# Kernel optimization log

Hardware: AMD Instinct MI355X
Metric: run time of the kernel (lower is better)

The kernel has to match this reference:

```python
import jax, jax.numpy as jnp
import numpy as np

N, L, DS, DP, H, A, Q, V = 1, 512, 384, 256, 12, 16, 4, 8
SHID = H * (DP + A + 3 * V + V)  # 3648
WC = float(np.sqrt(2.0 / (9.0 * Q)))
WL = float(np.sqrt(1.0 / 3.0))
EPS = 1e-5


def quat2rot(q):
    # q: (..., 3) partial quaternion (w fixed to 1, then normalized) -> (..., 3, 3)
    ones = jnp.ones(q.shape[:-1] + (1,), q.dtype)
    qf = jnp.concatenate([ones, q], axis=-1)
    qf = qf / jnp.linalg.norm(qf, axis=-1, keepdims=True)
    w, x, y, z = qf[..., 0], qf[..., 1], qf[..., 2], qf[..., 3]
    r0 = jnp.stack([1 - 2 * (y * y + z * z), 2 * (x * y - w * z), 2 * (x * z + w * y)], -1)
    r1 = jnp.stack([2 * (x * y + w * z), 1 - 2 * (x * x + z * z), 2 * (y * z - w * x)], -1)
    r2 = jnp.stack([2 * (x * z - w * y), 2 * (y * z + w * x), 1 - 2 * (x * x + y * y)], -1)
    return jnp.stack([r0, r1, r2], axis=-2)


def layer_norm(x, g, b):
    m = x.mean(-1, keepdims=True)
    v = ((x - m) ** 2).mean(-1, keepdims=True)
    return (x - m) / jnp.sqrt(v + EPS) * g + b


def setup_inputs() -> dict:
    key = jax.random.key(0)
    ks = jax.random.split(key, 24)
    w = lambda k, shape, s=0.02: (jax.random.normal(k, shape, jnp.float32) * s)
    return {
        'sfea': jax.random.normal(ks[0], (N, L, DS), jnp.float32),
        'pfea': jax.random.normal(ks[1], (N, L, L, DP), jnp.float32),
        'quat': jax.random.normal(ks[2], (N, L, 3), jnp.float32) * 0.1,
        'trsl': jax.random.normal(ks[3], (N, L, 3), jnp.float32),
        'Wq': w(ks[4], (DS, H * A)), 'Wk': w(ks[5], (DS, H * A)), 'Wv': w(ks[6], (DS, H * A)),
        'Wqp': w(ks[7], (DS, H * Q * 3)), 'Wkp': w(ks[8], (DS, H * Q * 3)), 'Wvp': w(ks[9], (DS, H * V * 3)),
        'Wb': w(ks[10], (DP, H)),
        'scale': jnp.ones((H,), jnp.float32),
        'Ws': w(ks[11], (SHID, DS)), 'bs': jnp.zeros((DS,), jnp.float32),
        'W1': w(ks[12], (DS, DS)), 'b1': jnp.zeros((DS,), jnp.float32),
        'W2': w(ks[13], (DS, DS)), 'b2': jnp.zeros((DS,), jnp.float32),
        'W3': w(ks[14], (DS, DS)), 'b3': jnp.zeros((DS,), jnp.float32),
        'g1': jnp.ones((DS,), jnp.float32), 'be1': jnp.zeros((DS,), jnp.float32),
        'g2': jnp.ones((DS,), jnp.float32), 'be2': jnp.zeros((DS,), jnp.float32),
    }


def reference(sfea, pfea, quat, trsl, Wq, Wk, Wv, Wqp, Wkp, Wvp, Wb, scale, Ws, bs,
              W1, b1, W2, b2, W3, b3, g1, be1, g2, be2):
    n, l = sfea.shape[0], sfea.shape[1]
    # projections
    q = (sfea @ Wq).reshape(n, l, H, A)
    k = (sfea @ Wk).reshape(n, l, H, A)
    v = (sfea @ Wv).reshape(n, l, H, A)
    qp = (sfea @ Wqp).reshape(n, l, H, Q, 3)
    kp = (sfea @ Wkp).reshape(n, l, H, Q, 3)
    vp = (sfea @ Wvp).reshape(n, l, H, V, 3)
    b = jnp.einsum('nijp,ph->nijh', pfea, Wb)
    # local frames
    rot = quat2rot(quat)  # (n, l, 3, 3)
    t = trsl[:, :, None, None, :]
    qp_g = jnp.einsum('nlij,nlhqj->nlhqi', rot, qp) + t
    kp_g = jnp.einsum('nlij,nlhqj->nlhqi', rot, kp) + t
    vp_g = jnp.einsum('nlij,nlhvj->nlhvi', rot, vp) + t
    # attention logits
    qk = jnp.einsum('nihd,njhd->nijh', q, k) / np.sqrt(A)
    diff = qp_g[:, :, None] - kp_g[:, None]  # (n, i, j, h, q, 3)
    d2 = jnp.sum(diff * diff, axis=(-1, -2))  # (n, i, j, h)
    qkp = (WC * jax.nn.softplus(scale) / 2.0) * d2
    a = jax.nn.softmax(WL * (qk + b - qkp), axis=2)  # (n, i, j, h)
    # weighted sums (einsum avoids huge broadcast intermediates)
    op = jnp.einsum('nijh,nijp->nihp', a, pfea)
    ov = jnp.einsum('nijh,njhd->nihd', a, v)
    ovp_g = jnp.einsum('nijh,njhvc->nihvc', a, vp_g)
    # map back into local frame: R^T (x - t)
    ovp = jnp.einsum('nlji,nlhvj->nlhvi', rot, ovp_g - t)
    ovp_norm = jnp.sqrt(jnp.sum(ovp * ovp, axis=-1))  # (n, l, h, v)
    shid = jnp.concatenate([op, ov, ovp.reshape(n, l, H, V * 3), ovp_norm], axis=-1)
    shid = shid.reshape(n, l, SHID)
    # output projection + residual, post-LN, MLP, post-LN (v1 path, p_drop=0)
    s = sfea + shid @ Ws + bs
    s = layer_norm(s, g1, be1)
    h = jax.nn.relu(s @ W1 + b1)
    h = jax.nn.relu(h @ W2 + b2)
    s = s + (h @ W3 + b3)
    s = layer_norm(s, g2, be2)
    return s
```

## Files before the change

### kernel.cpp

```cpp
#include <hip/hip_runtime.h>
#include <cstddef>

typedef __attribute__((ext_vector_type(8))) short short8;
typedef __attribute__((ext_vector_type(4))) float f32x4;

#define WC_CONST 0.2357022603955158f
#define WL_CONST 0.5773502691896258f

__device__ __forceinline__ unsigned short rne_bf16(float f) {
  unsigned int u = __float_as_uint(f);
  u += 0x7fffu + ((u >> 16) & 1u);
  return (unsigned short)(u >> 16);
}

__global__ __launch_bounds__(256) void concat_w_kernel(
    const float* __restrict__ Wq, const float* __restrict__ Wk, const float* __restrict__ Wv,
    const float* __restrict__ Wqp, const float* __restrict__ Wkp, const float* __restrict__ Wvp,
    float* __restrict__ Wcat) {
  int idx = blockIdx.x * 256 + threadIdx.x;
  if (idx >= 384 * 1152) return;
  int k = idx / 1152, c = idx % 1152;
  float v;
  if (c < 192)       v = Wq [k*192 + c];
  else if (c < 384)  v = Wk [k*192 + (c-192)];
  else if (c < 576)  v = Wv [k*192 + (c-384)];
  else if (c < 720)  v = Wqp[k*144 + (c-576)];
  else if (c < 864)  v = Wkp[k*144 + (c-720)];
  else               v = Wvp[k*288 + (c-864)];
  Wcat[idx] = v;
}

__global__ __launch_bounds__(256) void gemm64_kernel(
    const float* __restrict__ Amat, const float* __restrict__ Bmat, float* __restrict__ Cp,
    int M, int N, int K, int ksl) {
  __shared__ float As[16][68];
  __shared__ float Bs[16][68];
  int t = threadIdx.x;
  int bn = blockIdx.x, bm = blockIdx.y, bz = blockIdx.z;
  int k0 = bz * ksl;
  int tr = t >> 4, tc = t & 15;
  int lm = t >> 2, lk4 = (t & 3) << 2;
  int lkb = t >> 4, lnq = (t & 15) << 2;
  const float* Ab = Amat + (size_t)(bm*64 + lm) * K;
  const float* Bb = Bmat + bn*64 + lnq;
  float acc[4][4];
  #pragma unroll
  for (int a2 = 0; a2 < 4; a2++)
    #pragma unroll
    for (int b2 = 0; b2 < 4; b2++) acc[a2][b2] = 0.f;

  for (int k = k0; k < k0 + ksl; k += 16) {
    float4 av = *(const float4*)(Ab + k + lk4);
    float4 bv = *(const float4*)(Bb + (size_t)(k + lkb) * N);
    As[lk4+0][lm] = av.x; As[lk4+1][lm] = av.y; As[lk4+2][lm] = av.z; As[lk4+3][lm] = av.w;
    *(float4*)&Bs[lkb][lnq] = bv;
    __syncthreads();
    #pragma unroll
    for (int kk = 0; kk < 16; kk++) {
      float4 a4 = *(const float4*)&As[kk][tr << 2];
      float4 b4 = *(const float4*)&Bs[kk][tc << 2];
      float ar[4] = {a4.x, a4.y, a4.z, a4.w};
      float br[4] = {b4.x, b4.y, b4.z, b4.w};
      #pragma unroll
      for (int a2 = 0; a2 < 4; a2++)
        #pragma unroll
        for (int b2 = 0; b2 < 4; b2++) acc[a2][b2] += ar[a2] * br[b2];
    }
    __syncthreads();
  }
  float* Cb = Cp + (size_t)bz * M * N + (size_t)(bm*64 + (tr << 2)) * N + bn*64 + (tc << 2);
  #pragma unroll
  for (int r = 0; r < 4; r++) {
    float4 o = {acc[r][0], acc[r][1], acc[r][2], acc[r][3]};
    *(float4*)(Cb + (size_t)r * N) = o;
  }
}

__global__ __launch_bounds__(256) void reduce_kernel(
    const float* __restrict__ Cp, float* __restrict__ out, const float* __restrict__ bias,
    int relu, int MN, int N, int sk) {
  int idx = blockIdx.x * 256 + threadIdx.x;
  if (idx >= MN) return;
  float s = 0.f;
  for (int z = 0; z < sk; z++) s += Cp[(size_t)z * MN + idx];
  if (bias) s += bias[idx % N];
  if (relu) s = fmaxf(s, 0.f);
  out[idx] = s;
}

__global__ __launch_bounds__(64) void frames_kernel(
    const float* __restrict__ proj, const float* __restrict__ quat, const float* __restrict__ trsl,
    float* __restrict__ rotb, float* __restrict__ qpg, float* __restrict__ kpg,
    float* __restrict__ vpg) {
  int i = blockIdx.x, t = threadIdx.x;
  float q0 = quat[i*3+0], q1 = quat[i*3+1], q2 = quat[i*3+2];
  float inv = rsqrtf(1.f + q0*q0 + q1*q1 + q2*q2);
  float w = inv, x = q0*inv, y = q1*inv, z = q2*inv;
  float R00 = 1.f - 2.f*(y*y + z*z), R01 = 2.f*(x*y - w*z), R02 = 2.f*(x*z + w*y);
  float R10 = 2.f*(x*y + w*z), R11 = 1.f - 2.f*(x*x + z*z), R12 = 2.f*(y*z - w*x);
  float R20 = 2.f*(x*z - w*y), R21 = 2.f*(y*z + w*x), R22 = 1.f - 2.f*(x*x + y*y);
  float t0 = trsl[i*3+0], t1 = trsl[i*3+1], t2 = trsl[i*3+2];
  if (t == 0) {
    float* rb = rotb + i*9;
    rb[0]=R00; rb[1]=R01; rb[2]=R02; rb[3]=R10; rb[4]=R11; rb[5]=R12; rb[6]=R20; rb[7]=R21; rb[8]=R22;
  }
  for (int pt = t; pt < 192; pt += 64) {
    const float* src; float* dst;
    if (pt < 48)      { src = proj + i*1152 + 576 + pt*3;        dst = qpg + i*144 + pt*3; }
    else if (pt < 96) { src = proj + i*1152 + 720 + (pt-48)*3;   dst = kpg + i*144 + (pt-48)*3; }
    else              { src = proj + i*1152 + 864 + (pt-96)*3;   dst = vpg + i*288 + (pt-96)*3; }
    float p0 = src[0], p1 = src[1], p2 = src[2];
    dst[0] = R00*p0 + R01*p1 + R02*p2 + t0;
    dst[1] = R10*p0 + R11*p1 + R12*p2 + t1;
    dst[2] = R20*p0 + R21*p1 + R22*p2 + t2;
  }
}

__global__ __launch_bounds__(256) void b_mfma_kernel(
    const float* __restrict__ pfea, const float* __restrict__ Wb, float* __restrict__ bmat) {
  __shared__ short wbf[8][64][8];
  int t = threadIdx.x;
  for (int s = t; s < 512; s += 256) {
    int ks = s >> 6, l = s & 63;
    int col = l & 15, kb = ks * 32 + ((l >> 4) << 3);
    #pragma unroll
    for (int j = 0; j < 8; j++)
      wbf[ks][l][j] = (col < 12) ? (short)rne_bf16(Wb[(kb + j) * 12 + col]) : (short)0;
  }
  __syncthreads();
  int wv = t >> 6, lane = t & 63;
  int wglob = blockIdx.x * 4 + wv;
  int row = lane & 15, kq = lane >> 4;
  for (int it = 0; it < 4; it++) {
    int tile = wglob * 4 + it;
    size_t p0 = (size_t)tile * 16;
    const float* Ab = pfea + (p0 + row) * 256 + kq * 8;
    f32x4 acc = {0.f, 0.f, 0.f, 0.f};
    #pragma unroll
    for (int ks = 0; ks < 8; ks++) {
      float4 f0 = *(const float4*)(Ab + ks * 32);
      float4 f1 = *(const float4*)(Ab + ks * 32 + 4);
      short8 af;
      af[0] = (short)rne_bf16(f0.x); af[1] = (short)rne_bf16(f0.y);
      af[2] = (short)rne_bf16(f0.z); af[3] = (short)rne_bf16(f0.w);
      af[4] = (short)rne_bf16(f1.x); af[5] = (short)rne_bf16(f1.y);
      af[6] = (short)rne_bf16(f1.z); af[7] = (short)rne_bf16(f1.w);
      short8 bfv = *(const short8*)(&wbf[ks][lane][0]);
      acc = __builtin_amdgcn_mfma_f32_16x16x32_bf16(af, bfv, acc, 0, 0, 0);
    }
    int col = lane & 15;
    if (col < 12) {
      #pragma unroll
      for (int r = 0; r < 4; r++) {
        size_t pr = p0 + kq * 4 + r;
        bmat[pr * 12 + col] = acc[r];
      }
    }
  }
}

__global__ __launch_bounds__(768) void attn_kernel(
    const float* __restrict__ proj, const float* __restrict__ qpg,
    const float* __restrict__ kpg, const float* __restrict__ vpg,
    const float* __restrict__ bmat, const float* __restrict__ pfea,
    const float* __restrict__ rotb, const float* __restrict__ trsl,
    const float* __restrict__ scale, float* __restrict__ shid) {
  int i = blockIdx.x;
  int t = threadIdx.x;
  __shared__ float Ll[12][512];
  __shared__ float qs[12][16];
  __shared__ float qps[12][12];
  __shared__ float coefs[12];
  __shared__ float ovpg_l[12][24];
  __shared__ float rot_s[9];

  for (int idx = t; idx < 192; idx += 768) qs[idx >> 4][idx & 15] = proj[i*1152 + idx];
  for (int idx = t; idx < 144; idx += 768) qps[idx / 12][idx % 12] = qpg[i*144 + idx];
  if (t < 12) coefs[t] = WC_CONST * 0.5f * log1pf(__expf(scale[t]));
  if (t < 9)  rot_s[t] = rotb[i*9 + t];
  __syncthreads();

  for (int idx = t; idx < 6144; idx += 768) {
    int h = idx % 12, j = idx / 12;
    const float4* kr = (const float4*)(proj + j*1152 + 192 + h*16);
    const float4* qr = (const float4*)(&qs[h][0]);
    float qk = 0.f;
    #pragma unroll
    for (int m = 0; m < 4; m++) {
      float4 kv = kr[m], qv = qr[m];
      qk += qv.x*kv.x + qv.y*kv.y + qv.z*kv.z + qv.w*kv.w;
    }
    const float4* kpr = (const float4*)(kpg + j*144 + h*12);
    const float4* qpr = (const float4*)(&qps[h][0]);
    float d2 = 0.f;
    #pragma unroll
    for (int m = 0; m < 3; m++) {
      float4 kv = kpr[m], qv = qpr[m];
      float dx = qv.x-kv.x, dy = qv.y-kv.y, dz = qv.z-kv.z, dw = qv.w-kv.w;
      d2 += dx*dx + dy*dy + dz*dz + dw*dw;
    }
    Ll[h][j] = WL_CONST * (qk*0.25f + bmat[(size_t)(i*512 + j)*12 + h] - coefs[h]*d2);
  }
  __syncthreads();

  int w = t >> 6, lane = t & 63;
  {
    float vals[8];
    float m = -1e30f;
    #pragma unroll
    for (int r = 0; r < 8; r++) { vals[r] = Ll[w][lane + (r<<6)]; m = fmaxf(m, vals[r]); }
    #pragma unroll
    for (int off = 32; off >= 1; off >>= 1) m = fmaxf(m, __shfl_xor(m, off));
    float s = 0.f;
    #pragma unroll
    for (int r = 0; r < 8; r++) { vals[r] = __expf(vals[r] - m); s += vals[r]; }
    #pragma unroll
    for (int off = 32; off >= 1; off >>= 1) s += __shfl_xor(s, off);
    float invs = 1.0f / s;
    #pragma unroll
    for (int r = 0; r < 8; r++) Ll[w][lane + (r<<6)] = vals[r] * invs;
  }
  __syncthreads();

  {
    float4 acc = {0.f, 0.f, 0.f, 0.f};
    const float* pf = pfea + (size_t)i * 131072 + (lane << 2);
    #pragma unroll 2
    for (int j = 0; j < 512; j += 4) {
      float4 av = *(const float4*)&Ll[w][j];
      const float* pj = pf + (size_t)j * 256;
      float4 r0 = *(const float4*)(pj);
      float4 r1 = *(const float4*)(pj + 256);
      float4 r2 = *(const float4*)(pj + 512);
      float4 r3 = *(const float4*)(pj + 768);
      acc.x += av.x*r0.x + av.y*r1.x + av.z*r2.x + av.w*r3.x;
      acc.y += av.x*r0.y + av.y*r1.y + av.z*r2.y + av.w*r3.y;
      acc.z += av.x*r0.z + av.y*r1.z + av.z*r2.z + av.w*r3.z;
      acc.w += av.x*r0.w + av.y*r1.w + av.z*r2.w + av.w*r3.w;
    }
    *(float4*)(shid + (size_t)i*3648 + w*304 + (lane << 2)) = acc;
  }

  if (t < 192) {
    int h = t >> 4, d = t & 15;
    const float* vb = proj + 384 + h*16 + d;
    float acc = 0.f;
    #pragma unroll 8
    for (int j = 0; j < 512; j++) acc += Ll[h][j] * vb[(size_t)j * 1152];
    shid[(size_t)i*3648 + h*304 + 256 + d] = acc;
  } else if (t >= 256 && t < 544) {
    int idx = t - 256, h = idx / 24, m2 = idx % 24;
    const float* vb = vpg + h*24 + m2;
    float acc = 0.f;
    #pragma unroll 8
    for (int j = 0; j < 512; j++) acc += Ll[h][j] * vb[(size_t)j * 288];
    ovpg_l[h][m2] = acc;
  }
  __syncthreads();

  if (t < 96) {
    int h = t >> 3, vv = t & 7;
    float x = ovpg_l[h][vv*3+0] - trsl[i*3+0];
    float y = ovpg_l[h][vv*3+1] - trsl[i*3+1];
    float z = ovpg_l[h][vv*3+2] - trsl[i*3+2];
    float o0 = rot_s[0]*x + rot_s[3]*y + rot_s[6]*z;
    float o1 = rot_s[1]*x + rot_s[4]*y + rot_s[7]*z;
    float o2 = rot_s[2]*x + rot_s[5]*y + rot_s[8]*z;
    float* so = shid + (size_t)i*3648 + h*304 + 272 + vv*3;
    so[0] = o0; so[1] = o1; so[2] = o2;
    shid[(size_t)i*3648 + h*304 + 296 + vv] = sqrtf(o0*o0 + o1*o1 + o2*o2);
  }
}

__global__ __launch_bounds__(384) void ln384_kernel(
    const float* __restrict__ resid, const float* __restrict__ C, const float* __restrict__ bias,
    const float* __restrict__ g, const float* __restrict__ be, float* __restrict__ out) {
  int i = blockIdx.x, t = threadIdx.x;
  __shared__ float red[6];
  float x = resid[(size_t)i*384 + t] + C[(size_t)i*384 + t] + bias[t];
  float s = x;
  #pragma unroll
  for (int off = 32; off >= 1; off >>= 1) s += __shfl_xor(s, off);
  if ((t & 63) == 0) red[t >> 6] = s;
  __syncthreads();
  float m = (red[0]+red[1]+red[2]+red[3]+red[4]+red[5]) * (1.f/384.f);
  __syncthreads();
  float d = x - m;
  float v = d * d;
  #pragma unroll
  for (int off = 32; off >= 1; off >>= 1) v += __shfl_xor(v, off);
  if ((t & 63) == 0) red[t >> 6] = v;
  __syncthreads();
  float var = (red[0]+red[1]+red[2]+red[3]+red[4]+red[5]) * (1.f/384.f);
  out[(size_t)i*384 + t] = d * rsqrtf(var + 1e-5f) * g[t] + be[t];
}

extern "C" void kernel_launch(void* const* d_in, const int* in_sizes, int n_in,
                              void* d_out, int out_size, void* d_ws, size_t ws_size,
                              hipStream_t stream) {
  const float* sfea = (const float*)d_in[0];
  const float* pfea = (const float*)d_in[1];
  const float* quat = (const float*)d_in[2];
  const float* trsl = (const float*)d_in[3];
  const float* Wq   = (const float*)d_in[4];
  const float* Wk   = (const float*)d_in[5];
  const float* Wv   = (const float*)d_in[6];
  const float* Wqp  = (const float*)d_in[7];
  const float* Wkp  = (const float*)d_in[8];
  const float* Wvp  = (const float*)d_in[9];
  const float* Wb   = (const float*)d_in[10];
  const float* scale= (const float*)d_in[11];
  const float* Wsm  = (const float*)d_in[12];
  const float* bs   = (const float*)d_in[13];
  const float* W1   = (const float*)d_in[14];
  const float* b1   = (const float*)d_in[15];
  const float* W2   = (const float*)d_in[16];
  const float* b2   = (const float*)d_in[17];
  const float* W3   = (const float*)d_in[18];
  const float* b3   = (const float*)d_in[19];
  const float* g1   = (const float*)d_in[20];
  const float* be1  = (const float*)d_in[21];
  const float* g2   = (const float*)d_in[22];
  const float* be2  = (const float*)d_in[23];
  float* out = (float*)d_out;
  float* wsf = (float*)d_ws;

  float* Wcat = wsf;
  float* proj = Wcat + 442368;
  float* rotb = proj + 589824;
  float* qpg  = rotb + 4608;
  float* kpg  = qpg + 73728;
  float* vpg  = kpg + 73728;
  float* bmat = vpg + 147456;
  float* shid = bmat + 3145728;
  float* cpart= shid + 1867776;
  float* C1   = cpart + 1179648;
  float* s1   = C1 + 196608;
  float* h1   = s1 + 196608;
  float* h2   = h1 + 196608;
  float* C3   = h2 + 196608;

  concat_w_kernel<<<1728, 256, 0, stream>>>(Wq, Wk, Wv, Wqp, Wkp, Wvp, Wcat);
  gemm64_kernel<<<dim3(18, 8, 1), 256, 0, stream>>>(sfea, Wcat, proj, 512, 1152, 384, 384);
  frames_kernel<<<512, 64, 0, stream>>>(proj, quat, trsl, rotb, qpg, kpg, vpg);
  b_mfma_kernel<<<1024, 256, 0, stream>>>(pfea, Wb, bmat);
  attn_kernel<<<512, 768, 0, stream>>>(proj, qpg, kpg, vpg, bmat, pfea, rotb, trsl, scale, shid);

  gemm64_kernel<<<dim3(6, 8, 6), 256, 0, stream>>>(shid, Wsm, cpart, 512, 384, 3648, 608);
  reduce_kernel<<<768, 256, 0, stream>>>(cpart, C1, nullptr, 0, 196608, 384, 6);
  ln384_kernel<<<512, 384, 0, stream>>>(sfea, C1, bs, g1, be1, s1);

  gemm64_kernel<<<dim3(6, 8, 3), 256, 0, stream>>>(s1, W1, cpart, 512, 384, 384, 128);
  reduce_kernel<<<768, 256, 0, stream>>>(cpart, h1, b1, 1, 196608, 384, 3);
  gemm64_kernel<<<dim3(6, 8, 3), 256, 0, stream>>>(h1, W2, cpart, 512, 384, 384, 128);
  reduce_kernel<<<768, 256, 0, stream>>>(cpart, h2, b2, 1, 196608, 384, 3);
  gemm64_kernel<<<dim3(6, 8, 3), 256, 0, stream>>>(h2, W3, cpart, 512, 384, 384, 128);
  reduce_kernel<<<768, 256, 0, stream>>>(cpart, C3, nullptr, 0, 196608, 384, 3);
  ln384_kernel<<<512, 384, 0, stream>>>(s1, C3, b3, g2, be2, out);
}
```

Measured before the change: 366.0 us.

## Fuse pair-bias MFMA into attention kernel with single-pass pfea streaming

Removes the separate bias kernel and instead streams each row's pfea through shared memory in 32-row chunks, using it both for the bf16 MFMA bias projection and for the attention-weighted pair-feature sum. Warps are specialised: some compute the bias MFMA, some prefetch the next chunk's query-key logits, and some load the next pfea chunk into registers. Softmax becomes unnormalised exponentials with a deferred sum, so pfea (the dominant traffic) is read once instead of twice and the bmat round trip is dropped. In exchange there are more block barriers, a 12-head register accumulator per thread, a cross-warp reduction, and no max subtraction in the exponent, which can overflow for large logits.

```diff
diff --git a/kernel.cpp b/kernel.cpp
--- a/kernel.cpp
+++ b/kernel.cpp
@@ -116,145 +116,198 @@
   }
 }
 
-__global__ __launch_bounds__(256) void b_mfma_kernel(
-    const float* __restrict__ pfea, const float* __restrict__ Wb, float* __restrict__ bmat) {
-  __shared__ short wbf[8][64][8];
-  int t = threadIdx.x;
-  for (int s = t; s < 512; s += 256) {
-    int ks = s >> 6, l = s & 63;
-    int col = l & 15, kb = ks * 32 + ((l >> 4) << 3);
-    #pragma unroll
-    for (int j = 0; j < 8; j++)
-      wbf[ks][l][j] = (col < 12) ? (short)rne_bf16(Wb[(kb + j) * 12 + col]) : (short)0;
-  }
-  __syncthreads();
-  int wv = t >> 6, lane = t & 63;
-  int wglob = blockIdx.x * 4 + wv;
-  int row = lane & 15, kq = lane >> 4;
-  for (int it = 0; it < 4; it++) {
-    int tile = wglob * 4 + it;
-    size_t p0 = (size_t)tile * 16;
-    const float* Ab = pfea + (p0 + row) * 256 + kq * 8;
-    f32x4 acc = {0.f, 0.f, 0.f, 0.f};
-    #pragma unroll
-    for (int ks = 0; ks < 8; ks++) {
-      float4 f0 = *(const float4*)(Ab + ks * 32);
-      float4 f1 = *(const float4*)(Ab + ks * 32 + 4);
-      short8 af;
-      af[0] = (short)rne_bf16(f0.x); af[1] = (short)rne_bf16(f0.y);
-      af[2] = (short)rne_bf16(f0.z); af[3] = (short)rne_bf16(f0.w);
-      af[4] = (short)rne_bf16(f1.x); af[5] = (short)rne_bf16(f1.y);
-      af[6] = (short)rne_bf16(f1.z); af[7] = (short)rne_bf16(f1.w);
-      short8 bfv = *(const short8*)(&wbf[ks][lane][0]);
-      acc = __builtin_amdgcn_mfma_f32_16x16x32_bf16(af, bfv, acc, 0, 0, 0);
-    }
-    int col = lane & 15;
-    if (col < 12) {
-      #pragma unroll
-      for (int r = 0; r < 4; r++) {
-        size_t pr = p0 + kq * 4 + r;
-        bmat[pr * 12 + col] = acc[r];
-      }
-    }
-  }
-}
-
-__global__ __launch_bounds__(768) void attn_kernel(
+__device__ __forceinline__ float lt1_val(
+    const float* __restrict__ proj, const float* __restrict__ kpg,
+    const float* qs_, const float* qps_, float coef, int jg, int h) {
+  const float4* kr = (const float4*)(proj + (size_t)jg*1152 + 192 + h*16);
+  const float4* qr = (const float4*)(qs_ + h*16);
+  float qk = 0.f;
+  #pragma unroll
+  for (int m = 0; m < 4; m++) {
+    float4 kv = kr[m], qv = qr[m];
+    qk += qv.x*kv.x + qv.y*kv.y + qv.z*kv.z + qv.w*kv.w;
+  }
+  const float4* kpr = (const float4*)(kpg + (size_t)jg*144 + h*12);
+  const float4* qpr = (const float4*)(qps_ + h*12);
+  float d2 = 0.f;
+  #pragma unroll
+  for (int m = 0; m < 3; m++) {
+    float4 kv = kpr[m], qv = qpr[m];
+    float dx = qv.x-kv.x, dy = qv.y-kv.y, dz = qv.z-kv.z, dw = qv.w-kv.w;
+    d2 += dx*dx + dy*dy + dz*dz + dw*dw;
+  }
+  return qk*0.25f - coef*d2;
+}
+
+__global__ __launch_bounds__(768) void attn2_kernel(
     const float* __restrict__ proj, const float* __restrict__ qpg,
     const float* __restrict__ kpg, const float* __restrict__ vpg,
-    const float* __restrict__ bmat, const float* __restrict__ pfea,
+    const float* __restrict__ pfea, const float* __restrict__ Wb,
     const float* __restrict__ rotb, const float* __restrict__ trsl,
     const float* __restrict__ scale, float* __restrict__ shid) {
+  __shared__ __align__(16) float P[32][260];
+  __shared__ __align__(16) float Lw[512][12];
+  __shared__ short wbf[8][64][8];
+  __shared__ float Lb[2][32][12];
+  __shared__ __align__(16) float qs[12][16];
+  __shared__ __align__(16) float qps[12][12];
+  __shared__ float coefs[12];
+  __shared__ float sh_inv[12];
+  __shared__ float rot_s[9];
+  __shared__ float ovpg_l[12][24];
+
   int i = blockIdx.x;
   int t = threadIdx.x;
-  __shared__ float Ll[12][512];
-  __shared__ float qs[12][16];
-  __shared__ float qps[12][12];
-  __shared__ float coefs[12];
-  __shared__ float ovpg_l[12][24];
-  __shared__ float rot_s[9];
+  int w = t >> 6, lane = t & 63;
 
   for (int idx = t; idx < 192; idx += 768) qs[idx >> 4][idx & 15] = proj[i*1152 + idx];
   for (int idx = t; idx < 144; idx += 768) qps[idx / 12][idx % 12] = qpg[i*144 + idx];
   if (t < 12) coefs[t] = WC_CONST * 0.5f * log1pf(__expf(scale[t]));
   if (t < 9)  rot_s[t] = rotb[i*9 + t];
-  __syncthreads();
-
-  for (int idx = t; idx < 6144; idx += 768) {
-    int h = idx % 12, j = idx / 12;
-    const float4* kr = (const float4*)(proj + j*1152 + 192 + h*16);
-    const float4* qr = (const float4*)(&qs[h][0]);
-    float qk = 0.f;
-    #pragma unroll
-    for (int m = 0; m < 4; m++) {
-      float4 kv = kr[m], qv = qr[m];
-      qk += qv.x*kv.x + qv.y*kv.y + qv.z*kv.z + qv.w*kv.w;
+  for (int s2 = t; s2 < 512; s2 += 768) {
+    int ks = s2 >> 6, l = s2 & 63;
+    int col = l & 15, kb = ks * 32 + ((l >> 4) << 3);
+    #pragma unroll
+    for (int j = 0; j < 8; j++)
+      wbf[ks][l][j] = (col < 12) ? (short)rne_bf16(Wb[(kb + j) * 12 + col]) : (short)0;
+  }
+  __syncthreads();
+
+  float4 opacc[12];
+  #pragma unroll
+  for (int h = 0; h < 12; h++) { opacc[h].x = 0.f; opacc[h].y = 0.f; opacc[h].z = 0.f; opacc[h].w = 0.f; }
+  float4 streg[8];
+
+  if (w >= 8) {
+    int rbase = (w - 8) * 8;
+    const float* src = pfea + (size_t)i * 131072;
+    #pragma unroll
+    for (int q2 = 0; q2 < 8; q2++)
+      streg[q2] = *(const float4*)(src + (size_t)(rbase + q2) * 256 + (lane << 2));
+  } else if (w >= 2) {
+    int e = (w - 2) * 64 + lane;
+    int jl = e / 12, h = e - jl * 12;
+    Lb[0][jl][h] = lt1_val(proj, kpg, &qs[0][0], &qps[0][0], coefs[h], jl, h);
+  }
+
+  for (int tt = 0; tt < 16; tt++) {
+    __syncthreads();
+    if (w >= 8) {
+      int rbase = (w - 8) * 8;
+      #pragma unroll
+      for (int q2 = 0; q2 < 8; q2++)
+        *(float4*)&P[rbase + q2][lane << 2] = streg[q2];
     }
-    const float4* kpr = (const float4*)(kpg + j*144 + h*12);
-    const float4* qpr = (const float4*)(&qps[h][0]);
-    float d2 = 0.f;
-    #pragma unroll
-    for (int m = 0; m < 3; m++) {
-      float4 kv = kpr[m], qv = qpr[m];
-      float dx = qv.x-kv.x, dy = qv.y-kv.y, dz = qv.z-kv.z, dw = qv.w-kv.w;
-      d2 += dx*dx + dy*dy + dz*dz + dw*dw;
+    __syncthreads();
+    if (w < 2) {
+      f32x4 accb = {0.f, 0.f, 0.f, 0.f};
+      int row = (w << 4) + (lane & 15);
+      int kq = lane >> 4;
+      const float* Pb = &P[row][kq * 8];
+      #pragma unroll
+      for (int ks = 0; ks < 8; ks++) {
+        float4 f0 = *(const float4*)(Pb + ks * 32);
+        float4 f1 = *(const float4*)(Pb + ks * 32 + 4);
+        short8 af;
+        af[0] = (short)rne_bf16(f0.x); af[1] = (short)rne_bf16(f0.y);
+        af[2] = (short)rne_bf16(f0.z); af[3] = (short)rne_bf16(f0.w);
+        af[4] = (short)rne_bf16(f1.x); af[5] = (short)rne_bf16(f1.y);
+        af[6] = (short)rne_bf16(f1.z); af[7] = (short)rne_bf16(f1.w);
+        short8 bfv = *(const short8*)(&wbf[ks][lane][0]);
+        accb = __builtin_amdgcn_mfma_f32_16x16x32_bf16(af, bfv, accb, 0, 0, 0);
+      }
+      int h = lane & 15;
+      if (h < 12) {
+        #pragma unroll
+        for (int r = 0; r < 4; r++) {
+          int jl = (w << 4) + kq * 4 + r;
+          float lv = Lb[tt & 1][jl][h] + accb[r];
+          Lw[tt * 32 + jl][h] = __expf(WL_CONST * lv);
+        }
+      }
+    } else if (w < 8) {
+      if (tt < 15) {
+        int e = (w - 2) * 64 + lane;
+        int jl = e / 12, h = e - jl * 12;
+        Lb[(tt + 1) & 1][jl][h] =
+            lt1_val(proj, kpg, &qs[0][0], &qps[0][0], coefs[h], (tt + 1) * 32 + jl, h);
+      }
+    } else {
+      if (tt < 15) {
+        int rbase = (w - 8) * 8;
+        const float* src = pfea + (size_t)i * 131072 + (size_t)(tt + 1) * 32 * 256;
+        #pragma unroll
+        for (int q2 = 0; q2 < 8; q2++)
+          streg[q2] = *(const float4*)(src + (size_t)(rbase + q2) * 256 + (lane << 2));
+      }
     }
-    Ll[h][j] = WL_CONST * (qk*0.25f + bmat[(size_t)(i*512 + j)*12 + h] - coefs[h]*d2);
-  }
-  __syncthreads();
-
-  int w = t >> 6, lane = t & 63;
-  {
-    float vals[8];
-    float m = -1e30f;
-    #pragma unroll
-    for (int r = 0; r < 8; r++) { vals[r] = Ll[w][lane + (r<<6)]; m = fmaxf(m, vals[r]); }
-    #pragma unroll
-    for (int off = 32; off >= 1; off >>= 1) m = fmaxf(m, __shfl_xor(m, off));
-    float s = 0.f;
-    #pragma unroll
-    for (int r = 0; r < 8; r++) { vals[r] = __expf(vals[r] - m); s += vals[r]; }
-    #pragma unroll
-    for (int off = 32; off >= 1; off >>= 1) s += __shfl_xor(s, off);
-    float invs = 1.0f / s;
-    #pragma unroll
-    for (int r = 0; r < 8; r++) Ll[w][lane + (r<<6)] = vals[r] * invs;
-  }
-  __syncthreads();
-
-  {
-    float4 acc = {0.f, 0.f, 0.f, 0.f};
-    const float* pf = pfea + (size_t)i * 131072 + (lane << 2);
-    #pragma unroll 2
-    for (int j = 0; j < 512; j += 4) {
-      float4 av = *(const float4*)&Ll[w][j];
-      const float* pj = pf + (size_t)j * 256;
-      float4 r0 = *(const float4*)(pj);
-      float4 r1 = *(const float4*)(pj + 256);
-      float4 r2 = *(const float4*)(pj + 512);
-      float4 r3 = *(const float4*)(pj + 768);
-      acc.x += av.x*r0.x + av.y*r1.x + av.z*r2.x + av.w*r3.x;
-      acc.y += av.x*r0.y + av.y*r1.y + av.z*r2.y + av.w*r3.y;
-      acc.z += av.x*r0.z + av.y*r1.z + av.z*r2.z + av.w*r3.z;
-      acc.w += av.x*r0.w + av.y*r1.w + av.z*r2.w + av.w*r3.w;
+    __syncthreads();
+    for (int rr = w; rr < 32; rr += 12) {
+      const float4* lwp = (const float4*)&Lw[tt * 32 + rr][0];
+      float4 wa = lwp[0], wb2 = lwp[1], wc = lwp[2];
+      float4 pv = *(const float4*)&P[rr][lane << 2];
+      opacc[0].x += pv.x*wa.x; opacc[0].y += pv.y*wa.x; opacc[0].z += pv.z*wa.x; opacc[0].w += pv.w*wa.x;
+      opacc[1].x += pv.x*wa.y; opacc[1].y += pv.y*wa.y; opacc[1].z += pv.z*wa.y; opacc[1].w += pv.w*wa.y;
+      opacc[2].x += pv.x*wa.z; opacc[2].y += pv.y*wa.z; opacc[2].z += pv.z*wa.z; opacc[2].w += pv.w*wa.z;
+      opacc[3].x += pv.x*wa.w; opacc[3].y += pv.y*wa.w; opacc[3].z += pv.z*wa.w; opacc[3].w += pv.w*wa.w;
+      opacc[4].x += pv.x*wb2.x; opacc[4].y += pv.y*wb2.x; opacc[4].z += pv.z*wb2.x; opacc[4].w += pv.w*wb2.x;
+      opacc[5].x += pv.x*wb2.y; opacc[5].y += pv.y*wb2.y; opacc[5].z += pv.z*wb2.y; opacc[5].w += pv.w*wb2.y;
+      opacc[6].x += pv.x*wb2.z; opacc[6].y += pv.y*wb2.z; opacc[6].z += pv.z*wb2.z; opacc[6].w += pv.w*wb2.z;
+      opacc[7].x += pv.x*wb2.w; opacc[7].y += pv.y*wb2.w; opacc[7].z += pv.z*wb2.w; opacc[7].w += pv.w*wb2.w;
+      opacc[8].x += pv.x*wc.x; opacc[8].y += pv.y*wc.x; opacc[8].z += pv.z*wc.x; opacc[8].w += pv.w*wc.x;
+      opacc[9].x += pv.x*wc.y; opacc[9].y += pv.y*wc.y; opacc[9].z += pv.z*wc.y; opacc[9].w += pv.w*wc.y;
+      opacc[10].x += pv.x*wc.z; opacc[10].y += pv.y*wc.z; opacc[10].z += pv.z*wc.z; opacc[10].w += pv.w*wc.z;
+      opacc[11].x += pv.x*wc.w; opacc[11].y += pv.y*wc.w; opacc[11].z += pv.z*wc.w; opacc[11].w += pv.w*wc.w;
     }
-    *(float4*)(shid + (size_t)i*3648 + w*304 + (lane << 2)) = acc;
+  }
+  __syncthreads();
+
+  if (w < 12) {
+    float sacc = 0.f;
+    #pragma unroll
+    for (int r2 = 0; r2 < 8; r2++) sacc += Lw[r2 * 64 + lane][w];
+    #pragma unroll
+    for (int off = 32; off >= 1; off >>= 1) sacc += __shfl_xor(sacc, off);
+    if (lane == 0) sh_inv[w] = 1.0f / sacc;
+  }
+  __syncthreads();
+
+  float4* Pred = (float4*)&P[0][0];
+  #pragma unroll
+  for (int gr = 0; gr < 6; gr++) {
+    Pred[(w * 2 + 0) * 64 + lane] = opacc[2 * gr + 0];
+    Pred[(w * 2 + 1) * 64 + lane] = opacc[2 * gr + 1];
+    __syncthreads();
+    if (t < 128) {
+      int hh = t >> 6, ll = t & 63;
+      float4 sum = {0.f, 0.f, 0.f, 0.f};
+      #pragma unroll
+      for (int w2 = 0; w2 < 12; w2++) {
+        float4 v = Pred[(w2 * 2 + hh) * 64 + ll];
+        sum.x += v.x; sum.y += v.y; sum.z += v.z; sum.w += v.w;
+      }
+      int h = 2 * gr + hh;
+      float isv = sh_inv[h];
+      float4 o = {sum.x * isv, sum.y * isv, sum.z * isv, sum.w * isv};
+      *(float4*)(shid + (size_t)i * 3648 + h * 304 + (ll << 2)) = o;
+    }
+    __syncthreads();
   }
 
   if (t < 192) {
     int h = t >> 4, d = t & 15;
-    const float* vb = proj + 384 + h*16 + d;
+    const float* vb = proj + 384 + h * 16 + d;
     float acc = 0.f;
     #pragma unroll 8
-    for (int j = 0; j < 512; j++) acc += Ll[h][j] * vb[(size_t)j * 1152];
-    shid[(size_t)i*3648 + h*304 + 256 + d] = acc;
+    for (int j = 0; j < 512; j++) acc += Lw[j][h] * vb[(size_t)j * 1152];
+    shid[(size_t)i * 3648 + h * 304 + 256 + d] = acc * sh_inv[h];
   } else if (t >= 256 && t < 544) {
     int idx = t - 256, h = idx / 24, m2 = idx % 24;
-    const float* vb = vpg + h*24 + m2;
+    const float* vb = vpg + h * 24 + m2;
     float acc = 0.f;
     #pragma unroll 8
-    for (int j = 0; j < 512; j++) acc += Ll[h][j] * vb[(size_t)j * 288];
-    ovpg_l[h][m2] = acc;
+    for (int j = 0; j < 512; j++) acc += Lw[j][h] * vb[(size_t)j * 288];
+    ovpg_l[h][m2] = acc * sh_inv[h];
   }
   __syncthreads();
 
@@ -331,8 +384,7 @@
   float* qpg  = rotb + 4608;
   float* kpg  = qpg + 73728;
   float* vpg  = kpg + 73728;
-  float* bmat = vpg + 147456;
-  float* shid = bmat + 3145728;
+  float* shid = vpg + 147456;
   float* cpart= shid + 1867776;
   float* C1   = cpart + 1179648;
   float* s1   = C1 + 196608;
@@ -343,8 +395,7 @@
   concat_w_kernel<<<1728, 256, 0, stream>>>(Wq, Wk, Wv, Wqp, Wkp, Wvp, Wcat);
   gemm64_kernel<<<dim3(18, 8, 1), 256, 0, stream>>>(sfea, Wcat, proj, 512, 1152, 384, 384);
   frames_kernel<<<512, 64, 0, stream>>>(proj, quat, trsl, rotb, qpg, kpg, vpg);
-  b_mfma_kernel<<<1024, 256, 0, stream>>>(pfea, Wb, bmat);
-  attn_kernel<<<512, 768, 0, stream>>>(proj, qpg, kpg, vpg, bmat, pfea, rotb, trsl, scale, shid);
+  attn2_kernel<<<512, 768, 0, stream>>>(proj, qpg, kpg, vpg, pfea, Wb, rotb, trsl, scale, shid);
 
   gemm64_kernel<<<dim3(6, 8, 6), 256, 0, stream>>>(shid, Wsm, cpart, 512, 384, 3648, 608);
   reduce_kernel<<<768, 256, 0, stream>>>(cpart, C1, nullptr, 0, 196608, 384, 6);
```

Result: faster. 308.0 us (-15.8%).
